# Kernel tuning notes

Measured on AMD Instinct MI355X. Metric: run time of the kernel, lower is better.

## Reference

```python
import jax, jax.numpy as jnp
import numpy as np

TEMPERATURE = 1.0
NEG = -1e9
EPS = 1e-8


def setup_inputs() -> dict:
    key = jax.random.key(0)
    k1, k2, k3 = jax.random.split(key, 3)
    B, H = 524288, 32
    scores = jax.random.normal(k1, (B, H), dtype=jnp.float32)
    rankings = jax.random.randint(k2, (B, H), 0, 33, dtype=jnp.int32)
    mask = jax.random.randint(k3, (B, H), 0, 2, dtype=jnp.int32).astype(bool)
    return {"scores": scores, "rankings": rankings, "mask": mask}


def reference(scores, rankings, mask):
    B, H = scores.shape
    # effective validity: horse present AND has a ranking > 0 (top_k=None)
    m = mask & (rankings > 0)
    # masked, temperature-scaled scores; -1e9 entries underflow to exactly 0 in softmax
    s = jnp.where(m, scores / TEMPERATURE, NEG)
    p = jax.nn.softmax(s, axis=1)  # [B, H], ~0 at invalid slots

    n_valid = jnp.sum(m, axis=1)  # [B]
    # ideal order: valid horses sorted by ranking ascending (invalid pushed to end)
    rank_key = jnp.where(m, rankings, jnp.iinfo(jnp.int32).max)
    rank_order = jnp.argsort(rank_key, axis=1)          # stable sort
    # prediction order: valid horses in original index order (matches torch.where)
    pos_order = jnp.argsort(~m, axis=1)                 # stable: valid first

    q = jnp.take_along_axis(p, rank_order, axis=1)      # ideal_probs, aligned by list position
    pr = jnp.take_along_axis(p, pos_order, axis=1)      # pred_probs,  aligned by list position

    # positions >= n_valid are padding
    valid_pos = jnp.arange(H)[None, :] < n_valid[:, None]
    q_safe = jnp.where(valid_pos, q, 1.0)
    pr_safe = jnp.where(valid_pos, pr, 1.0)
    # KL(ideal || pred) with the original's log(pred + 1e-8)
    kl_terms = q_safe * (jnp.log(q_safe) - jnp.log(pr_safe + EPS))
    kl = jnp.sum(jnp.where(valid_pos, kl_terms, 0.0), axis=1)  # [B]

    # rows with <= 1 valid ranked horse are skipped entirely
    row_ok = n_valid > 1
    n_rows = jnp.maximum(jnp.sum(row_ok), 1)
    return jnp.sum(jnp.where(row_ok, kl, 0.0)) / n_rows  # reduction='mean'
```

## Files before the change

kernel.cpp:

```cpp
#include <hip/hip_runtime.h>
#include <stdint.h>


#define H 32

__global__ __launch_bounds__(256, 4) void listwise_kernel(
    const float* __restrict__ scores,
    const int* __restrict__ rankings,
    const unsigned char* __restrict__ mask_u8,
    float* __restrict__ ws_kl,
    int* __restrict__ ws_cnt,
    int nrows)
{
    __shared__ float lds_row[256 * 33];
    __shared__ float s_kl[4];
    __shared__ int   s_cnt[4];

    const int tid  = threadIdx.x;
    const int lane = tid & 63;
    const int wid  = tid >> 6;
    const int row  = blockIdx.x * 256 + tid;

    unsigned char probe = mask_u8[lane];
    const bool mask_is_i32 =
        (__ballot(((lane & 3) != 0) && (probe != 0)) == 0ull);

    float th_kl = 0.0f;
    int   th_cnt = 0;

    if (row < nrows) {
        float s[H];
        {
            const float4* p = (const float4*)(scores + (size_t)row * H);
            #pragma unroll
            for (int c = 0; c < H / 4; ++c) {
                float4 v = p[c];
                s[4*c+0] = v.x; s[4*c+1] = v.y; s[4*c+2] = v.z; s[4*c+3] = v.w;
            }
        }
        int r[H];
        {
            const int4* p = (const int4*)(rankings + (size_t)row * H);
            #pragma unroll
            for (int c = 0; c < H / 4; ++c) {
                int4 v = p[c];
                r[4*c+0] = v.x; r[4*c+1] = v.y; r[4*c+2] = v.z; r[4*c+3] = v.w;
            }
        }

        uint32_t vbits = 0;
        if (mask_is_i32) {
            const int4* p = (const int4*)((const int*)mask_u8 + (size_t)row * H);
            #pragma unroll
            for (int c = 0; c < H / 4; ++c) {
                int4 v = p[c];
                vbits |= (v.x != 0 ? 1u : 0u) << (4*c+0);
                vbits |= (v.y != 0 ? 1u : 0u) << (4*c+1);
                vbits |= (v.z != 0 ? 1u : 0u) << (4*c+2);
                vbits |= (v.w != 0 ? 1u : 0u) << (4*c+3);
            }
        } else {
            const uint4* p = (const uint4*)(mask_u8 + (size_t)row * H);
            #pragma unroll
            for (int c = 0; c < 2; ++c) {
                uint4 v = p[c];
                uint32_t w[4] = {v.x, v.y, v.z, v.w};
                #pragma unroll
                for (int q = 0; q < 4; ++q)
                    #pragma unroll
                    for (int b = 0; b < 4; ++b)
                        vbits |= ((((w[q] >> (8*b)) & 0xFFu) != 0u) ? 1u : 0u)
                                 << (16*c + 4*q + b);
            }
        }

        uint32_t key[H];
        int nv = 0;
        #pragma unroll
        for (int k = 0; k < H; ++k) {
            const bool valid = (((vbits >> k) & 1u) != 0u) && (r[k] > 0);
            key[k] = valid ? ((((uint32_t)r[k]) << 5) | (uint32_t)k)
                           : (0x10000u | (uint32_t)k);
            nv += valid ? 1 : 0;
        }

        float* rowp = &lds_row[tid * 33];
        int jp = 0;
        #pragma unroll
        for (int k = 0; k < H; ++k) {
            const bool valid = key[k] < 0x10000u;
            rowp[valid ? jp : 32] = s[k];
            jp += valid ? 1 : 0;
        }

        float se = 0.0f, num = 0.0f;
        #pragma unroll
        for (int i = 0; i < H; ++i) {
            int j = 0;
            #pragma unroll
            for (int k = 0; k < H; ++k) j += (key[k] < key[i]) ? 1 : 0;
            const float g = rowp[j];
            const float e = __expf(s[i]);
            const bool valid = key[i] < 0x10000u;
            se += valid ? e : 0.0f;
            const float t = e * (s[i] - g);
            num += valid ? t : 0.0f;
        }
        if (nv > 1) { th_kl = __fdividef(num, se); th_cnt = 1; }
    }

    #pragma unroll
    for (int m = 32; m >= 1; m >>= 1) {
        th_kl  += __shfl_xor(th_kl, m);
        th_cnt += __shfl_xor(th_cnt, m);
    }
    if (lane == 0) { s_kl[wid] = th_kl; s_cnt[wid] = th_cnt; }
    __syncthreads();
    if (tid == 0) {
        atomicAdd(ws_kl,  s_kl[0] + s_kl[1] + s_kl[2] + s_kl[3]);
        atomicAdd(ws_cnt, s_cnt[0] + s_cnt[1] + s_cnt[2] + s_cnt[3]);
    }
}

__global__ void finalize_kernel(const float* __restrict__ ws_kl,
                                const int* __restrict__ ws_cnt,
                                float* __restrict__ out)
{
    if (threadIdx.x == 0) {
        int c = *ws_cnt;
        if (c < 1) c = 1;
        out[0] = *ws_kl / (float)c;
    }
}

extern "C" void kernel_launch(void* const* d_in, const int* in_sizes, int n_in,
                              void* d_out, int out_size, void* d_ws, size_t ws_size,
                              hipStream_t stream) {
    const float* scores = (const float*)d_in[0];
    const int* rankings = (const int*)d_in[1];
    const unsigned char* mask = (const unsigned char*)d_in[2];
    float* out = (float*)d_out;

    const int total = in_sizes[0];
    const int nrows = total / H;

    float* wsf = (float*)d_ws;
    int*   wsi = (int*)d_ws;

    hipMemsetAsync(d_ws, 0, 8, stream);

    const int threads = 256;
    const int blocks = (nrows + threads - 1) / threads;
    listwise_kernel<<<blocks, threads, 0, stream>>>(
        scores, rankings, mask, wsf, wsi + 1, nrows);

    finalize_kernel<<<1, 64, 0, stream>>>(wsf, wsi + 1, out);
}
```

Before: 216.5 us.

## Store gathered scores as bf16 in LDS and replace atomics with per-block partials

The sorted-score LDS buffer now holds bf16 (upper 16 bits, rounded) instead of fp32, which halves LDS use per block so more blocks can be resident. Loads are interleaved: rankings are read and turned into keys, then scores are read and scattered in the same loop, which reduces register pressure. The global atomics and memset are replaced by per-block partial sums that a 256-thread finalize kernel reduces. The bf16 gather adds rounding error to the KL terms.

```diff
diff --git a/kernel.cpp b/kernel.cpp
--- a/kernel.cpp
+++ b/kernel.cpp
@@ -3,56 +3,36 @@
 
 
 #define H 32
+#define BLK 256
 
-__global__ __launch_bounds__(256, 4) void listwise_kernel(
+__global__ __launch_bounds__(BLK, 4) void listwise_kernel(
     const float* __restrict__ scores,
     const int* __restrict__ rankings,
     const unsigned char* __restrict__ mask_u8,
-    float* __restrict__ ws_kl,
-    int* __restrict__ ws_cnt,
+    float* __restrict__ part_kl,
+    float* __restrict__ part_cnt,
     int nrows)
 {
-    __shared__ float lds_row[256 * 33];
-    __shared__ float s_kl[4];
-    __shared__ int   s_cnt[4];
+    __shared__ unsigned short lds[BLK * 34];
+    __shared__ float s_kl[4], s_cnt[4];
 
     const int tid  = threadIdx.x;
     const int lane = tid & 63;
     const int wid  = tid >> 6;
-    const int row  = blockIdx.x * 256 + tid;
+    const int row  = blockIdx.x * BLK + tid;
 
     unsigned char probe = mask_u8[lane];
     const bool mask_is_i32 =
         (__ballot(((lane & 3) != 0) && (probe != 0)) == 0ull);
 
-    float th_kl = 0.0f;
-    int   th_cnt = 0;
+    float kl = 0.0f, cnt = 0.0f;
 
     if (row < nrows) {
-        float s[H];
-        {
-            const float4* p = (const float4*)(scores + (size_t)row * H);
-            #pragma unroll
-            for (int c = 0; c < H / 4; ++c) {
-                float4 v = p[c];
-                s[4*c+0] = v.x; s[4*c+1] = v.y; s[4*c+2] = v.z; s[4*c+3] = v.w;
-            }
-        }
-        int r[H];
-        {
-            const int4* p = (const int4*)(rankings + (size_t)row * H);
-            #pragma unroll
-            for (int c = 0; c < H / 4; ++c) {
-                int4 v = p[c];
-                r[4*c+0] = v.x; r[4*c+1] = v.y; r[4*c+2] = v.z; r[4*c+3] = v.w;
-            }
-        }
-
         uint32_t vbits = 0;
         if (mask_is_i32) {
             const int4* p = (const int4*)((const int*)mask_u8 + (size_t)row * H);
             #pragma unroll
-            for (int c = 0; c < H / 4; ++c) {
+            for (int c = 0; c < 8; ++c) {
                 int4 v = p[c];
                 vbits |= (v.x != 0 ? 1u : 0u) << (4*c+0);
                 vbits |= (v.y != 0 ? 1u : 0u) << (4*c+1);
@@ -76,21 +56,42 @@
 
         uint32_t key[H];
         int nv = 0;
-        #pragma unroll
-        for (int k = 0; k < H; ++k) {
-            const bool valid = (((vbits >> k) & 1u) != 0u) && (r[k] > 0);
-            key[k] = valid ? ((((uint32_t)r[k]) << 5) | (uint32_t)k)
-                           : (0x10000u | (uint32_t)k);
-            nv += valid ? 1 : 0;
+        {
+            const int4* p = (const int4*)(rankings + (size_t)row * H);
+            #pragma unroll
+            for (int c = 0; c < 8; ++c) {
+                int4 v = p[c];
+                int rr[4] = {v.x, v.y, v.z, v.w};
+                #pragma unroll
+                for (int q = 0; q < 4; ++q) {
+                    const int k = 4*c + q;
+                    const bool valid =
+                        (((vbits >> k) & 1u) != 0u) && (rr[q] > 0);
+                    key[k] = valid ? ((((uint32_t)rr[q]) << 5) | (uint32_t)k)
+                                   : (0x800u | (uint32_t)k);
+                    nv += valid ? 1 : 0;
+                }
+            }
         }
 
-        float* rowp = &lds_row[tid * 33];
-        int jp = 0;
-        #pragma unroll
-        for (int k = 0; k < H; ++k) {
-            const bool valid = key[k] < 0x10000u;
-            rowp[valid ? jp : 32] = s[k];
-            jp += valid ? 1 : 0;
+        float s[H];
+        unsigned short* rowp = &lds[tid * 34];
+        {
+            const float4* p = (const float4*)(scores + (size_t)row * H);
+            int jp = 0;
+            #pragma unroll
+            for (int c = 0; c < 8; ++c) {
+                float4 v = p[c];
+                s[4*c+0] = v.x; s[4*c+1] = v.y; s[4*c+2] = v.z; s[4*c+3] = v.w;
+                #pragma unroll
+                for (int q = 0; q < 4; ++q) {
+                    const int k = 4*c + q;
+                    const bool valid = key[k] < 0x800u;
+                    const uint32_t b = __float_as_uint(s[k]) + 0x8000u;
+                    rowp[valid ? jp : 32] = (unsigned short)(b >> 16);
+                    jp += valid ? 1 : 0;
+                }
+            }
         }
 
         float se = 0.0f, num = 0.0f;
@@ -99,37 +100,54 @@
             int j = 0;
             #pragma unroll
             for (int k = 0; k < H; ++k) j += (key[k] < key[i]) ? 1 : 0;
-            const float g = rowp[j];
-            const float e = __expf(s[i]);
-            const bool valid = key[i] < 0x10000u;
-            se += valid ? e : 0.0f;
-            const float t = e * (s[i] - g);
-            num += valid ? t : 0.0f;
+            const float g = __uint_as_float(((uint32_t)rowp[j]) << 16);
+            const bool valid = key[i] < 0x800u;
+            float e = __expf(s[i]);
+            e = valid ? e : 0.0f;
+            const float d = valid ? (s[i] - g) : 0.0f;
+            se += e;
+            num = __builtin_fmaf(e, d, num);
         }
-        if (nv > 1) { th_kl = __fdividef(num, se); th_cnt = 1; }
+        if (nv > 1) { kl = __fdividef(num, se); cnt = 1.0f; }
     }
 
     #pragma unroll
     for (int m = 32; m >= 1; m >>= 1) {
-        th_kl  += __shfl_xor(th_kl, m);
-        th_cnt += __shfl_xor(th_cnt, m);
+        kl  += __shfl_xor(kl, m);
+        cnt += __shfl_xor(cnt, m);
     }
-    if (lane == 0) { s_kl[wid] = th_kl; s_cnt[wid] = th_cnt; }
+    if (lane == 0) { s_kl[wid] = kl; s_cnt[wid] = cnt; }
     __syncthreads();
     if (tid == 0) {
-        atomicAdd(ws_kl,  s_kl[0] + s_kl[1] + s_kl[2] + s_kl[3]);
-        atomicAdd(ws_cnt, s_cnt[0] + s_cnt[1] + s_cnt[2] + s_cnt[3]);
+        part_kl[blockIdx.x]  = s_kl[0] + s_kl[1] + s_kl[2] + s_kl[3];
+        part_cnt[blockIdx.x] = s_cnt[0] + s_cnt[1] + s_cnt[2] + s_cnt[3];
     }
 }
 
-__global__ void finalize_kernel(const float* __restrict__ ws_kl,
-                                const int* __restrict__ ws_cnt,
-                                float* __restrict__ out)
+__global__ __launch_bounds__(256) void finalize_kernel(
+    const float* __restrict__ part_kl,
+    const float* __restrict__ part_cnt,
+    float* __restrict__ out, int nblk)
 {
+    float k = 0.0f, c = 0.0f;
+    for (int i = threadIdx.x; i < nblk; i += 256) {
+        k += part_kl[i];
+        c += part_cnt[i];
+    }
+    #pragma unroll
+    for (int m = 32; m >= 1; m >>= 1) {
+        k += __shfl_xor(k, m);
+        c += __shfl_xor(c, m);
+    }
+    __shared__ float sk[4], sc[4];
+    const int wid = threadIdx.x >> 6;
+    if ((threadIdx.x & 63) == 0) { sk[wid] = k; sc[wid] = c; }
+    __syncthreads();
     if (threadIdx.x == 0) {
-        int c = *ws_cnt;
-        if (c < 1) c = 1;
-        out[0] = *ws_kl / (float)c;
+        float K = sk[0] + sk[1] + sk[2] + sk[3];
+        float C = sc[0] + sc[1] + sc[2] + sc[3];
+        if (C < 1.0f) C = 1.0f;
+        out[0] = K / C;
     }
 }
 
@@ -143,16 +161,13 @@
 
     const int total = in_sizes[0];
     const int nrows = total / H;
+    const int blocks = (nrows + BLK - 1) / BLK;
 
-    float* wsf = (float*)d_ws;
-    int*   wsi = (int*)d_ws;
+    float* part_kl  = (float*)d_ws;
+    float* part_cnt = (float*)d_ws + blocks;
 
-    hipMemsetAsync(d_ws, 0, 8, stream);
+    listwise_kernel<<<blocks, BLK, 0, stream>>>(
+        scores, rankings, mask, part_kl, part_cnt, nrows);
 
-    const int threads = 256;
-    const int blocks = (nrows + threads - 1) / threads;
-    listwise_kernel<<<blocks, threads, 0, stream>>>(
-        scores, rankings, mask, wsf, wsi + 1, nrows);
-
-    finalize_kernel<<<1, 64, 0, stream>>>(wsf, wsi + 1, out);
+    finalize_kernel<<<1, 256, 0, stream>>>(part_kl, part_cnt, out, blocks);
 }
```

Result: no change. 215.5 us (-0.5%).
